# Optimization experiments

Hardware: AMD Instinct MI355X
Metric: run time of the kernel (lower is better)

Reference implementation:

```python
import jax, jax.numpy as jnp
import numpy as np

H = 256
K = 16
EPS_LN = 1e-5


def setup_inputs() -> dict:
    key = jax.random.key(0)
    ks = jax.random.split(key, 24)
    B, N = 64, 256
    s = lambda *sh: 1.0 / np.sqrt(sh[0])
    inp = {
        "feat": jax.random.normal(ks[0], (B, N, H), jnp.float32),
        "centers": jax.random.normal(ks[1], (B, N, 3), jnp.float32),
        "text_global": jax.random.normal(ks[2], (B, H), jnp.float32),
        # geom_mlp: Linear(4,H) -> ReLU -> Linear(H,H) -> ReLU
        "w_geom1": jax.random.normal(ks[3], (4, H), jnp.float32) * s(4),
        "b_geom1": jnp.zeros((H,), jnp.float32),
        "w_geom2": jax.random.normal(ks[4], (H, H), jnp.float32) * s(H),
        "b_geom2": jnp.zeros((H,), jnp.float32),
        # text gate / bias projections
        "w_gate": jax.random.normal(ks[5], (H, H), jnp.float32) * s(H),
        "b_gate": jnp.zeros((H,), jnp.float32),
        "w_tbias": jax.random.normal(ks[6], (H, H), jnp.float32) * s(H),
        "b_tbias": jnp.zeros((H,), jnp.float32),
        # edge_mlp: Linear(H,H//2) -> ReLU -> Linear(H//2,1)
        "w_edge1": jax.random.normal(ks[7], (H, H // 2), jnp.float32) * s(H),
        "b_edge1": jnp.zeros((H // 2,), jnp.float32),
        "w_edge2": jax.random.normal(ks[8], (H // 2, 1), jnp.float32) * s(H // 2),
        "b_edge2": jnp.zeros((1,), jnp.float32),
        # msg_mlp: Linear(H,H) -> ReLU
        "w_msg": jax.random.normal(ks[9], (H, H), jnp.float32) * s(H),
        "b_msg": jnp.zeros((H,), jnp.float32),
        # out_proj: Linear(2H,H) -> ReLU
        "w_out": jax.random.normal(ks[10], (2 * H, H), jnp.float32) * s(2 * H),
        "b_out": jnp.zeros((H,), jnp.float32),
        # LayerNorm params
        "ln_gamma": jnp.ones((H,), jnp.float32),
        "ln_beta": jnp.zeros((H,), jnp.float32),
    }
    return inp


def _forward(feat, centers, text_global,
             w_geom1, b_geom1, w_geom2, b_geom2,
             w_gate, b_gate, w_tbias, b_tbias,
             w_edge1, b_edge1, w_edge2, b_edge2,
             w_msg, b_msg, w_out, b_out, ln_gamma, ln_beta):
    B, N, Hd = feat.shape
    k = min(K, N)
    # pairwise euclidean distances (B,N,N)
    sq = jnp.sum(centers * centers, axis=-1)  # (B,N)
    d2 = sq[:, :, None] + sq[:, None, :] - 2.0 * jnp.einsum('bnc,bmc->bnm', centers, centers)
    dist_matrix = jnp.sqrt(jnp.maximum(d2, 0.0))
    # k smallest -> top_k of negated distances (sorted ascending in distance)
    _, knn_idx = jax.lax.top_k(-dist_matrix, k)  # (B,N,k)
    idx_flat = knn_idx.reshape(B, N * k)
    feat_neigh = jnp.take_along_axis(feat, idx_flat[:, :, None], axis=1).reshape(B, N, k, Hd)
    centers_neigh = jnp.take_along_axis(centers, idx_flat[:, :, None], axis=1).reshape(B, N, k, 3)
    rel = centers_neigh - centers[:, :, None, :]  # (B,N,k,3)
    dist = jnp.linalg.norm(rel, axis=-1, keepdims=True) + 1e-6
    geom = jnp.concatenate([rel, jnp.log1p(dist)], axis=-1)  # (B,N,k,4)
    geom_emb = jax.nn.relu(jax.nn.relu(geom @ w_geom1 + b_geom1) @ w_geom2 + b_geom2)
    text_gate = jax.nn.sigmoid(text_global @ w_gate + b_gate)[:, None, None, :]
    text_bias = (text_global @ w_tbias + b_tbias)[:, None, None, :]
    geom_cond = geom_emb * text_gate + text_bias
    edge_feat = jnp.tanh(feat[:, :, None, :] + feat_neigh + geom_cond)  # (B,N,k,H)
    edge_logits = (jax.nn.relu(edge_feat @ w_edge1 + b_edge1) @ w_edge2 + b_edge2)[..., 0]
    edge_alpha = jax.nn.softmax(edge_logits, axis=-1)[..., None]  # (B,N,k,1)
    msg = jax.nn.relu(feat_neigh @ w_msg + b_msg)
    ctx = jnp.sum(edge_alpha * msg, axis=2)  # (B,N,H)
    out = jax.nn.relu(jnp.concatenate([feat, ctx], axis=-1) @ w_out + b_out)
    x = feat + out
    mu = jnp.mean(x, axis=-1, keepdims=True)
    var = jnp.mean((x - mu) ** 2, axis=-1, keepdims=True)
    return (x - mu) / jnp.sqrt(var + EPS_LN) * ln_gamma + ln_beta


def reference(feat, centers, text_global,
              w_geom1, b_geom1, w_geom2, b_geom2,
              w_gate, b_gate, w_tbias, b_tbias,
              w_edge1, b_edge1, w_edge2, b_edge2,
              w_msg, b_msg, w_out, b_out, ln_gamma, ln_beta):
    return _forward(feat, centers, text_global,
                    w_geom1, b_geom1, w_geom2, b_geom2,
                    w_gate, b_gate, w_tbias, b_tbias,
                    w_edge1, b_edge1, w_edge2, b_edge2,
                    w_msg, b_msg, w_out, b_out, ln_gamma, ln_beta)
```

## Files before the change

kernel.cpp:

```cpp
#include <hip/hip_runtime.h>

#define H 256
#define KNN 16
#define NPT 256
#define BB 64

typedef unsigned short u16;
typedef unsigned int u32;
typedef __attribute__((ext_vector_type(8))) short shortx8;
typedef __attribute__((ext_vector_type(4))) float floatx4;

__device__ __forceinline__ u16 f2b(float f) {
    u32 u = __float_as_uint(f);
    u32 r = (u + 0x7fffu + ((u >> 16) & 1u)) >> 16;
    return (u16)r;
}

__device__ __forceinline__ float fast_tanh(float x) {
    float e = __builtin_amdgcn_exp2f(x * 2.88539008177793f);
    return 1.0f - 2.0f * __builtin_amdgcn_rcpf(e + 1.0f);
}

__global__ __launch_bounds__(256) void prep_kernel(
    const float* __restrict__ w2, const float* __restrict__ we1,
    const float* __restrict__ wm, const float* __restrict__ wo,
    const float* __restrict__ w1, const float* __restrict__ b1,
    u16* __restrict__ w2t, u16* __restrict__ we1t,
    u16* __restrict__ wmt, u16* __restrict__ wot, u16* __restrict__ w1t) {
    int tid = blockIdx.x * 256 + threadIdx.x;
    if (tid < 65536) {
        int n = tid >> 8, k = tid & 255;
        w2t[tid] = f2b(w2[k * 256 + n]);
    } else if (tid < 98304) {
        int t = tid - 65536;
        int n = t >> 8, k = t & 255;
        we1t[t] = f2b(we1[k * 128 + n]);
    } else if (tid < 163840) {
        int t = tid - 98304;
        int n = t >> 8, k = t & 255;
        wmt[t] = f2b(wm[k * 256 + n]);
    } else if (tid < 294912) {
        int t = tid - 163840;
        int n = t >> 9, k = t & 511;
        wot[t] = f2b(wo[k * 256 + n]);
    } else {
        int t = tid - 294912;
        int n = t >> 5, k = t & 31;
        float v = (k < 4) ? w1[k * 256 + n] : (k == 4 ? b1[n] : 0.0f);
        w1t[t] = f2b(v);
    }
}

__global__ __launch_bounds__(256) void knn_kernel(const float* __restrict__ centers,
                                                  int* __restrict__ knn) {
    __shared__ float cx[NPT], cy[NPT], cz[NPT], sq[NPT];
    __shared__ float dl[4][64][17];
    __shared__ int il[4][64][17];
    int blk = blockIdx.x;
    int b = blk >> 2, n0 = (blk & 3) * 64;
    int h = threadIdx.x;
    int s = h >> 6, pt = h & 63;
    {
        const float* cb = centers + (size_t)b * NPT * 3;
        float x = cb[h * 3 + 0], y = cb[h * 3 + 1], z = cb[h * 3 + 2];
        cx[h] = x; cy[h] = y; cz[h] = z;
        sq[h] = x * x + y * y + z * z;
    }
    __syncthreads();
    int n = n0 + pt;
    float x = cx[n], y = cy[n], z = cz[n], sn = sq[n];
    float bd[KNN];
    int bi[KNN];
#pragma unroll
    for (int j = 0; j < KNN; j++) { bd[j] = 1e30f; bi[j] = 0x7fffffff; }
    for (int mm = 0; mm < 64; mm++) {
        int m = s * 64 + mm;
        float dot = x * cx[m] + y * cy[m] + z * cz[m];
        float d2 = (sn + sq[m]) - 2.0f * dot;
        float d = sqrtf(fmaxf(d2, 0.0f));
        if (d < bd[KNN - 1]) {
            bd[KNN - 1] = d; bi[KNN - 1] = m;
#pragma unroll
            for (int p = KNN - 1; p > 0; --p) {
                if (bd[p - 1] > bd[p]) {
                    float td = bd[p - 1]; bd[p - 1] = bd[p]; bd[p] = td;
                    int ti = bi[p - 1]; bi[p - 1] = bi[p]; bi[p] = ti;
                }
            }
        }
    }
#pragma unroll
    for (int j = 0; j < KNN; j++) { dl[s][pt][j] = bd[j]; il[s][pt][j] = bi[j]; }
    __syncthreads();
    if (s == 0) {
        float md[KNN];
        int mi[KNN];
#pragma unroll
        for (int j = 0; j < KNN; j++) { md[j] = dl[0][pt][j]; mi[j] = il[0][pt][j]; }
        for (int t = 1; t < 4; t++) {
            for (int j = 0; j < KNN; j++) {
                float d = dl[t][pt][j];
                int idx = il[t][pt][j];
                bool ins = (d < md[KNN - 1]) || (d == md[KNN - 1] && idx < mi[KNN - 1]);
                if (!ins) break;
                md[KNN - 1] = d; mi[KNN - 1] = idx;
#pragma unroll
                for (int p = KNN - 1; p > 0; --p) {
                    bool sw = (md[p - 1] > md[p]) ||
                              (md[p - 1] == md[p] && mi[p - 1] > mi[p]);
                    if (sw) {
                        float td = md[p - 1]; md[p - 1] = md[p]; md[p] = td;
                        int ti = mi[p - 1]; mi[p - 1] = mi[p]; mi[p] = ti;
                    }
                }
            }
        }
        int* kp = knn + (b * NPT + n0 + pt) * KNN;
#pragma unroll
        for (int j = 0; j < KNN; j++) kp[j] = mi[j];
    }
}

__global__ __launch_bounds__(512) void gate_kernel(const float* __restrict__ tg_g,
                                                   const float* __restrict__ wg,
                                                   const float* __restrict__ bg,
                                                   const float* __restrict__ wtb,
                                                   const float* __restrict__ btb,
                                                   float* __restrict__ gate,
                                                   float* __restrict__ tbias) {
    __shared__ float tg[H];
    int b = blockIdx.x, t = threadIdx.x;
    if (t < H) tg[t] = tg_g[b * H + t];
    __syncthreads();
    int h = t & 255;
    if (t < H) {
        float ag = bg[h];
#pragma unroll 4
        for (int i = 0; i < H; i++) ag += tg[i] * wg[i * H + h];
        gate[b * H + h] = 1.0f / (1.0f + expf(-ag));
    } else {
        float ab = btb[h];
#pragma unroll 4
        for (int i = 0; i < H; i++) ab += tg[i] * wtb[i * H + h];
        tbias[b * H + h] = ab;
    }
}

__global__ __launch_bounds__(256, 4) void msg_mfma(const float* __restrict__ feat,
                                                   const u16* __restrict__ wmt,
                                                   const float* __restrict__ bm,
                                                   float* __restrict__ MSG) {
    __shared__ __attribute__((aligned(16))) u16 A[64][264];
    int p0 = blockIdx.x * 64, h = threadIdx.x;
    int w = h >> 6, lane = h & 63, quad = lane >> 4, lq = lane & 15;
#pragma unroll 8
    for (int row = 0; row < 64; row++)
        A[row][h] = f2b(feat[(size_t)(p0 + row) * H + h]);
    __syncthreads();
    floatx4 acc[4][4];
#pragma unroll
    for (int rt = 0; rt < 4; rt++)
#pragma unroll
        for (int ct = 0; ct < 4; ct++) acc[rt][ct] = (floatx4){0, 0, 0, 0};
#pragma unroll 2
    for (int kt = 0; kt < 8; kt++) {
        shortx8 bf[4];
#pragma unroll
        for (int ct = 0; ct < 4; ct++)
            bf[ct] = *(const shortx8*)&wmt[(w * 64 + ct * 16 + lq) * 256 + kt * 32 + quad * 8];
#pragma unroll
        for (int rt = 0; rt < 4; rt++) {
            shortx8 a = *(const shortx8*)&A[rt * 16 + lq][kt * 32 + quad * 8];
#pragma unroll
            for (int ct = 0; ct < 4; ct++)
                acc[rt][ct] = __builtin_amdgcn_mfma_f32_16x16x32_bf16(a, bf[ct], acc[rt][ct], 0, 0, 0);
        }
    }
#pragma unroll
    for (int ct = 0; ct < 4; ct++) {
        int col = w * 64 + ct * 16 + lq;
        float bmc = bm[col];
#pragma unroll
        for (int rt = 0; rt < 4; rt++)
#pragma unroll
            for (int r = 0; r < 4; r++) {
                int row = rt * 16 + quad * 4 + r;
                MSG[(size_t)(p0 + row) * H + col] = fmaxf(acc[rt][ct][r] + bmc, 0.0f);
            }
    }
}

__global__ __launch_bounds__(256, 4) void edge_mfma(
    const float* __restrict__ feat, const float* __restrict__ centers,
    const u16* __restrict__ w1t,
    const u16* __restrict__ w2t, const float* __restrict__ b2v,
    const u16* __restrict__ we1t, const float* __restrict__ be1,
    const float* __restrict__ we2, const float* __restrict__ be2,
    const int* __restrict__ knn, const float* __restrict__ gateG,
    const float* __restrict__ tbiasG, const float* __restrict__ MSG,
    float* __restrict__ ctxG) {
    __shared__ __attribute__((aligned(16))) u16 A[64][264];
    __shared__ float fnS[4][H];
    __shared__ __attribute__((aligned(16))) float geomS[64][4];
    __shared__ int nidxS[64];
    __shared__ float part[4][64];
    __shared__ float logitsS[64];
    __shared__ float alphaS[64];

    int bn0 = blockIdx.x * 4;
    int b = bn0 >> 8, n0 = bn0 & 255;
    int h = threadIdx.x;
    int w = h >> 6, lane = h & 63, quad = lane >> 4, lq = lane & 15;

    if (h < 64) nidxS[h] = knn[bn0 * KNN + h];
#pragma unroll
    for (int p = 0; p < 4; p++)
        fnS[p][h] = feat[(size_t)(bn0 + p) * H + h];
    if (h < 64) {
        int p = h >> 4;
        int m = nidxS[h];
        int n = n0 + p;
        const float* cb = centers + (size_t)b * NPT * 3;
        float rx = cb[m * 3 + 0] - cb[n * 3 + 0];
        float ry = cb[m * 3 + 1] - cb[n * 3 + 1];
        float rz = cb[m * 3 + 2] - cb[n * 3 + 2];
        float dist = sqrtf(rx * rx + ry * ry + rz * rz) + 1e-6f;
        geomS[h][0] = rx; geomS[h][1] = ry; geomS[h][2] = rz;
        geomS[h][3] = log1pf(dist);
    }
    __syncthreads();

    {
        shortx8 bw1[4];
#pragma unroll
        for (int ct = 0; ct < 4; ct++)
            bw1[ct] = *(const shortx8*)&w1t[(w * 64 + ct * 16 + lq) * 32 + quad * 8];
#pragma unroll
        for (int rt = 0; rt < 4; rt++) {
            shortx8 ag = {0, 0, 0, 0, 0, 0, 0, 0};
            if (quad == 0) {
                float4 g = *(const float4*)&geomS[rt * 16 + lq][0];
                ag[0] = (short)f2b(g.x);
                ag[1] = (short)f2b(g.y);
                ag[2] = (short)f2b(g.z);
                ag[3] = (short)f2b(g.w);
                ag[4] = (short)0x3F80;
            }
#pragma unroll
            for (int ct = 0; ct < 4; ct++) {
                floatx4 accg = __builtin_amdgcn_mfma_f32_16x16x32_bf16(
                    ag, bw1[ct], (floatx4){0, 0, 0, 0}, 0, 0, 0);
#pragma unroll
                for (int r = 0; r < 4; r++)
                    A[rt * 16 + quad * 4 + r][w * 64 + ct * 16 + lq] =
                        f2b(fmaxf(accg[r], 0.0f));
            }
        }
    }
    __syncthreads();

    floatx4 acc[4][4];
#pragma unroll
    for (int rt = 0; rt < 4; rt++)
#pragma unroll
        for (int ct = 0; ct < 4; ct++) acc[rt][ct] = (floatx4){0, 0, 0, 0};
#pragma unroll 2
    for (int kt = 0; kt < 8; kt++) {
        shortx8 bf[4];
#pragma unroll
        for (int ct = 0; ct < 4; ct++)
            bf[ct] = *(const shortx8*)&w2t[(w * 64 + ct * 16 + lq) * 256 + kt * 32 + quad * 8];
#pragma unroll
        for (int rt = 0; rt < 4; rt++) {
            shortx8 a = *(const shortx8*)&A[rt * 16 + lq][kt * 32 + quad * 8];
#pragma unroll
            for (int ct = 0; ct < 4; ct++)
                acc[rt][ct] = __builtin_amdgcn_mfma_f32_16x16x32_bf16(a, bf[ct], acc[rt][ct], 0, 0, 0);
        }
    }
    __syncthreads();

#pragma unroll
    for (int ct = 0; ct < 4; ct++) {
        int col = w * 64 + ct * 16 + lq;
        float b2c = b2v[col];
        float gc = gateG[b * H + col];
        float tc = tbiasG[b * H + col];
#pragma unroll
        for (int rt = 0; rt < 4; rt++) {
            float fnc = fnS[rt][col];
#pragma unroll
            for (int r = 0; r < 4; r++) {
                int row = rt * 16 + quad * 4 + r;
                float fb = feat[((size_t)b * NPT + nidxS[row]) * H + col];
                float emb = fmaxf(acc[rt][ct][r] + b2c, 0.0f);
                float ef = fast_tanh(fnc + fb + emb * gc + tc);
                A[row][col] = f2b(ef);
            }
        }
    }
    __syncthreads();

    floatx4 acc2[4][2];
#pragma unroll
    for (int rt = 0; rt < 4; rt++)
#pragma unroll
        for (int c2 = 0; c2 < 2; c2++) acc2[rt][c2] = (floatx4){0, 0, 0, 0};
#pragma unroll 2
    for (int kt = 0; kt < 8; kt++) {
        shortx8 bf[2];
#pragma unroll
        for (int c2 = 0; c2 < 2; c2++)
            bf[c2] = *(const shortx8*)&we1t[(w * 32 + c2 * 16 + lq) * 256 + kt * 32 + quad * 8];
#pragma unroll
        for (int rt = 0; rt < 4; rt++) {
            shortx8 a = *(const shortx8*)&A[rt * 16 + lq][kt * 32 + quad * 8];
#pragma unroll
            for (int c2 = 0; c2 < 2; c2++)
                acc2[rt][c2] = __builtin_amdgcn_mfma_f32_16x16x32_bf16(a, bf[c2], acc2[rt][c2], 0, 0, 0);
        }
    }

    float pl[4][4];
#pragma unroll
    for (int rt = 0; rt < 4; rt++)
#pragma unroll
        for (int r = 0; r < 4; r++) pl[rt][r] = 0.0f;
#pragma unroll
    for (int c2 = 0; c2 < 2; c2++) {
        int col = w * 32 + c2 * 16 + lq;
        float be1c = be1[col], w2c = we2[col];
#pragma unroll
        for (int rt = 0; rt < 4; rt++)
#pragma unroll
            for (int r = 0; r < 4; r++)
                pl[rt][r] += fmaxf(acc2[rt][c2][r] + be1c, 0.0f) * w2c;
    }
#pragma unroll
    for (int d = 1; d < 16; d <<= 1)
#pragma unroll
        for (int rt = 0; rt < 4; rt++)
#pragma unroll
            for (int r = 0; r < 4; r++) pl[rt][r] += __shfl_xor(pl[rt][r], d, 16);
    if (lq == 0) {
#pragma unroll
        for (int rt = 0; rt < 4; rt++)
#pragma unroll
            for (int r = 0; r < 4; r++)
                part[w][rt * 16 + quad * 4 + r] = pl[rt][r];
    }
    __syncthreads();
    if (h < 64)
        logitsS[h] = part[0][h] + part[1][h] + part[2][h] + part[3][h] + be2[0];
    __syncthreads();
    if (h < 64) {
        int base = (h >> 4) * 16;
        float mx = -1e30f;
#pragma unroll
        for (int j = 0; j < KNN; j++) mx = fmaxf(mx, logitsS[base + j]);
        float sum = 0.0f;
#pragma unroll
        for (int j = 0; j < KNN; j++) sum += expf(logitsS[base + j] - mx);
        alphaS[h] = expf(logitsS[h] - mx) / sum;
    }
    __syncthreads();

    {
        int p = h >> 6, cg = (h & 63) * 4;
        float4 c = {0, 0, 0, 0};
#pragma unroll
        for (int j = 0; j < KNN; j++) {
            float al = alphaS[p * 16 + j];
            float4 m = *(const float4*)&MSG[((size_t)b * NPT + nidxS[p * 16 + j]) * H + cg];
            c.x += al * m.x; c.y += al * m.y; c.z += al * m.z; c.w += al * m.w;
        }
        *(float4*)&ctxG[(size_t)(bn0 + p) * H + cg] = c;
    }
}

__global__ __launch_bounds__(256, 4) void out_mfma(const float* __restrict__ feat,
                                                   const float* __restrict__ ctxG,
                                                   const u16* __restrict__ wot,
                                                   const float* __restrict__ bo,
                                                   const float* __restrict__ gamma,
                                                   const float* __restrict__ beta,
                                                   float* __restrict__ out) {
    __shared__ __attribute__((aligned(16))) u16 A[32][520];
    __shared__ float redS[4][32], redS2[4][32];
    int p0 = blockIdx.x * 32, h = threadIdx.x;
    int w = h >> 6, lane = h & 63, quad = lane >> 4, lq = lane & 15;
#pragma unroll 8
    for (int row = 0; row < 32; row++) {
        A[row][h]       = f2b(feat[(size_t)(p0 + row) * H + h]);
        A[row][256 + h] = f2b(ctxG[(size_t)(p0 + row) * H + h]);
    }
    __syncthreads();
    floatx4 acc[2][4];
#pragma unroll
    for (int rt = 0; rt < 2; rt++)
#pragma unroll
        for (int ct = 0; ct < 4; ct++) acc[rt][ct] = (floatx4){0, 0, 0, 0};
#pragma unroll 2
    for (int kt = 0; kt < 16; kt++) {
        shortx8 bf[4];
#pragma unroll
        for (int ct = 0; ct < 4; ct++)
            bf[ct] = *(const shortx8*)&wot[(w * 64 + ct * 16 + lq) * 512 + kt * 32 + quad * 8];
#pragma unroll
        for (int rt = 0; rt < 2; rt++) {
            shortx8 a = *(const shortx8*)&A[rt * 16 + lq][kt * 32 + quad * 8];
#pragma unroll
            for (int ct = 0; ct < 4; ct++)
                acc[rt][ct] = __builtin_amdgcn_mfma_f32_16x16x32_bf16(a, bf[ct], acc[rt][ct], 0, 0, 0);
        }
    }
    float x[2][4][4];
    float sm[2][4], sq2[2][4];
#pragma unroll
    for (int rt = 0; rt < 2; rt++)
#pragma unroll
        for (int r = 0; r < 4; r++) { sm[rt][r] = 0.0f; sq2[rt][r] = 0.0f; }
#pragma unroll
    for (int rt = 0; rt < 2; rt++)
#pragma unroll
        for (int ct = 0; ct < 4; ct++) {
            int col = w * 64 + ct * 16 + lq;
            float boc = bo[col];
#pragma unroll
            for (int r = 0; r < 4; r++) {
                int row = rt * 16 + quad * 4 + r;
                float xx = feat[(size_t)(p0 + row) * H + col] +
                           fmaxf(acc[rt][ct][r] + boc, 0.0f);
                x[rt][ct][r] = xx;
                sm[rt][r] += xx;
                sq2[rt][r] += xx * xx;
            }
        }
#pragma unroll
    for (int d = 1; d < 16; d <<= 1)
#pragma unroll
        for (int rt = 0; rt < 2; rt++)
#pragma unroll
            for (int r = 0; r < 4; r++) {
                sm[rt][r] += __shfl_xor(sm[rt][r], d, 16);
                sq2[rt][r] += __shfl_xor(sq2[rt][r], d, 16);
            }
    if (lq == 0) {
#pragma unroll
        for (int rt = 0; rt < 2; rt++)
#pragma unroll
            for (int r = 0; r < 4; r++) {
                redS[w][rt * 16 + quad * 4 + r] = sm[rt][r];
                redS2[w][rt * 16 + quad * 4 + r] = sq2[rt][r];
            }
    }
    __syncthreads();
#pragma unroll
    for (int rt = 0; rt < 2; rt++)
#pragma unroll
        for (int r = 0; r < 4; r++) {
            int row = rt * 16 + quad * 4 + r;
            float s1 = redS[0][row] + redS[1][row] + redS[2][row] + redS[3][row];
            float s2 = redS2[0][row] + redS2[1][row] + redS2[2][row] + redS2[3][row];
            float mu = s1 * (1.0f / H);
            float var = s2 * (1.0f / H) - mu * mu;
            float inv = rsqrtf(fmaxf(var, 0.0f) + 1e-5f);
#pragma unroll
            for (int ct = 0; ct < 4; ct++) {
                int col = w * 64 + ct * 16 + lq;
                out[(size_t)(p0 + row) * H + col] =
                    (x[rt][ct][r] - mu) * inv * gamma[col] + beta[col];
            }
        }
}

extern "C" void kernel_launch(void* const* d_in, const int* in_sizes, int n_in,
                              void* d_out, int out_size, void* d_ws, size_t ws_size,
                              hipStream_t stream) {
    const float* feat    = (const float*)d_in[0];
    const float* centers = (const float*)d_in[1];
    const float* textg   = (const float*)d_in[2];
    const float* w1      = (const float*)d_in[3];
    const float* b1      = (const float*)d_in[4];
    const float* w2      = (const float*)d_in[5];
    const float* b2      = (const float*)d_in[6];
    const float* wg      = (const float*)d_in[7];
    const float* bg      = (const float*)d_in[8];
    const float* wtb     = (const float*)d_in[9];
    const float* btb     = (const float*)d_in[10];
    const float* we1     = (const float*)d_in[11];
    const float* be1     = (const float*)d_in[12];
    const float* we2     = (const float*)d_in[13];
    const float* be2     = (const float*)d_in[14];
    const float* wm      = (const float*)d_in[15];
    const float* bm      = (const float*)d_in[16];
    const float* wo      = (const float*)d_in[17];
    const float* bo      = (const float*)d_in[18];
    const float* gamma   = (const float*)d_in[19];
    const float* beta    = (const float*)d_in[20];

    char* ws = (char*)d_ws;
    size_t off = 0;
    int* knn     = (int*)(ws + off);   off += (size_t)BB * NPT * KNN * 4;
    float* gate  = (float*)(ws + off); off += (size_t)BB * H * 4;
    float* tbias = (float*)(ws + off); off += (size_t)BB * H * 4;
    float* MSG   = (float*)(ws + off); off += (size_t)BB * NPT * H * 4;
    float* ctxG  = (float*)(ws + off); off += (size_t)BB * NPT * H * 4;
    u16* w2t     = (u16*)(ws + off);   off += (size_t)256 * 256 * 2;
    u16* we1t    = (u16*)(ws + off);   off += (size_t)128 * 256 * 2;
    u16* wmt     = (u16*)(ws + off);   off += (size_t)256 * 256 * 2;
    u16* wot     = (u16*)(ws + off);   off += (size_t)256 * 512 * 2;
    u16* w1t     = (u16*)(ws + off);   off += (size_t)256 * 32 * 2;

    prep_kernel<<<1184, 256, 0, stream>>>(w2, we1, wm, wo, w1, b1,
                                          w2t, we1t, wmt, wot, w1t);
    knn_kernel<<<256, 256, 0, stream>>>(centers, knn);
    gate_kernel<<<BB, 512, 0, stream>>>(textg, wg, bg, wtb, btb, gate, tbias);
    msg_mfma<<<BB * NPT / 64, 256, 0, stream>>>(feat, wmt, bm, MSG);
    edge_mfma<<<BB * NPT / 4, 256, 0, stream>>>(feat, centers, w1t, w2t, b2,
                                                we1t, be1, we2, be2, knn, gate, tbias,
                                                MSG, ctxG);
    out_mfma<<<BB * NPT / 32, 256, 0, stream>>>(feat, ctxG, wot, bo, gamma, beta,
                                                (float*)d_out);
}
```

Before: 354.0 us.

## Store intermediates and feature copy in bf16 to halve memory traffic

Adds a bf16 copy of feat built in the prep kernel, and switches the MSG and ctx intermediate buffers from fp32 to bf16. The neighbour gathers in edge_mfma (feat and MSG rows) and the A-tile loads in msg_mfma and out_mfma now read half as many bytes. The aim is to cut global-memory and cache traffic on the gather-heavy edge kernel. It costs an extra pass over feat to convert it, and adds bf16 rounding to the neighbour features and the aggregated context.

Measured after the change: 347.3 us. About the same (-1.9%).

```diff
diff --git a/kernel.cpp b/kernel.cpp
--- a/kernel.cpp
+++ b/kernel.cpp
@@ -15,6 +15,9 @@
     u32 r = (u + 0x7fffu + ((u >> 16) & 1u)) >> 16;
     return (u16)r;
 }
+__device__ __forceinline__ float b2f(u16 u) {
+    return __uint_as_float(((u32)u) << 16);
+}
 
 __device__ __forceinline__ float fast_tanh(float x) {
     float e = __builtin_amdgcn_exp2f(x * 2.88539008177793f);
@@ -22,33 +25,45 @@
 }
 
 __global__ __launch_bounds__(256) void prep_kernel(
+    const float* __restrict__ feat,
     const float* __restrict__ w2, const float* __restrict__ we1,
     const float* __restrict__ wm, const float* __restrict__ wo,
     const float* __restrict__ w1, const float* __restrict__ b1,
     u16* __restrict__ w2t, u16* __restrict__ we1t,
-    u16* __restrict__ wmt, u16* __restrict__ wot, u16* __restrict__ w1t) {
-    int tid = blockIdx.x * 256 + threadIdx.x;
-    if (tid < 65536) {
-        int n = tid >> 8, k = tid & 255;
-        w2t[tid] = f2b(w2[k * 256 + n]);
-    } else if (tid < 98304) {
-        int t = tid - 65536;
-        int n = t >> 8, k = t & 255;
-        we1t[t] = f2b(we1[k * 128 + n]);
-    } else if (tid < 163840) {
-        int t = tid - 98304;
-        int n = t >> 8, k = t & 255;
-        wmt[t] = f2b(wm[k * 256 + n]);
-    } else if (tid < 294912) {
-        int t = tid - 163840;
-        int n = t >> 9, k = t & 511;
-        wot[t] = f2b(wo[k * 256 + n]);
-    } else {
-        int t = tid - 294912;
-        int n = t >> 5, k = t & 31;
-        float v = (k < 4) ? w1[k * 256 + n] : (k == 4 ? b1[n] : 0.0f);
-        w1t[t] = f2b(v);
-    }
+    u16* __restrict__ wmt, u16* __restrict__ wot, u16* __restrict__ w1t,
+    u16* __restrict__ featB) {
+    int blk = blockIdx.x;
+    if (blk < 1184) {
+        int tid = blk * 256 + threadIdx.x;
+        if (tid < 65536) {
+            int n = tid >> 8, k = tid & 255;
+            w2t[tid] = f2b(w2[k * 256 + n]);
+        } else if (tid < 98304) {
+            int t = tid - 65536;
+            int n = t >> 8, k = t & 255;
+            we1t[t] = f2b(we1[k * 128 + n]);
+        } else if (tid < 163840) {
+            int t = tid - 98304;
+            int n = t >> 8, k = t & 255;
+            wmt[t] = f2b(wm[k * 256 + n]);
+        } else if (tid < 294912) {
+            int t = tid - 163840;
+            int n = t >> 9, k = t & 511;
+            wot[t] = f2b(wo[k * 256 + n]);
+        } else {
+            int t = tid - 294912;
+            int n = t >> 5, k = t & 31;
+            float v = (k < 4) ? w1[k * 256 + n] : (k == 4 ? b1[n] : 0.0f);
+            w1t[t] = f2b(v);
+        }
+        return;
+    }
+    int e = (blk - 1184) * 256 + threadIdx.x;
+    float4 f = *(const float4*)&feat[(size_t)e * 4];
+    uint2 st;
+    st.x = (u32)f2b(f.x) | ((u32)f2b(f.y) << 16);
+    st.y = (u32)f2b(f.z) | ((u32)f2b(f.w) << 16);
+    *(uint2*)&featB[(size_t)e * 4] = st;
 }
 
 __global__ __launch_bounds__(256) void knn_kernel(const float* __restrict__ centers,
@@ -146,16 +161,16 @@
     }
 }
 
-__global__ __launch_bounds__(256, 4) void msg_mfma(const float* __restrict__ feat,
+__global__ __launch_bounds__(256, 4) void msg_mfma(const u16* __restrict__ featB,
                                                    const u16* __restrict__ wmt,
                                                    const float* __restrict__ bm,
-                                                   float* __restrict__ MSG) {
+                                                   u16* __restrict__ MSGB) {
     __shared__ __attribute__((aligned(16))) u16 A[64][264];
     int p0 = blockIdx.x * 64, h = threadIdx.x;
     int w = h >> 6, lane = h & 63, quad = lane >> 4, lq = lane & 15;
 #pragma unroll 8
     for (int row = 0; row < 64; row++)
-        A[row][h] = f2b(feat[(size_t)(p0 + row) * H + h]);
+        A[row][h] = featB[(size_t)(p0 + row) * H + h];
     __syncthreads();
     floatx4 acc[4][4];
 #pragma unroll
@@ -185,20 +200,21 @@
 #pragma unroll
             for (int r = 0; r < 4; r++) {
                 int row = rt * 16 + quad * 4 + r;
-                MSG[(size_t)(p0 + row) * H + col] = fmaxf(acc[rt][ct][r] + bmc, 0.0f);
+                MSGB[(size_t)(p0 + row) * H + col] = f2b(fmaxf(acc[rt][ct][r] + bmc, 0.0f));
             }
     }
 }
 
 __global__ __launch_bounds__(256, 4) void edge_mfma(
-    const float* __restrict__ feat, const float* __restrict__ centers,
+    const float* __restrict__ feat, const u16* __restrict__ featB,
+    const float* __restrict__ centers,
     const u16* __restrict__ w1t,
     const u16* __restrict__ w2t, const float* __restrict__ b2v,
     const u16* __restrict__ we1t, const float* __restrict__ be1,
     const float* __restrict__ we2, const float* __restrict__ be2,
     const int* __restrict__ knn, const float* __restrict__ gateG,
-    const float* __restrict__ tbiasG, const float* __restrict__ MSG,
-    float* __restrict__ ctxG) {
+    const float* __restrict__ tbiasG, const u16* __restrict__ MSGB,
+    u16* __restrict__ ctxB) {
     __shared__ __attribute__((aligned(16))) u16 A[64][264];
     __shared__ float fnS[4][H];
     __shared__ __attribute__((aligned(16))) float geomS[64][4];
@@ -292,7 +308,7 @@
 #pragma unroll
             for (int r = 0; r < 4; r++) {
                 int row = rt * 16 + quad * 4 + r;
-                float fb = feat[((size_t)b * NPT + nidxS[row]) * H + col];
+                float fb = b2f(featB[((size_t)b * NPT + nidxS[row]) * H + col]);
                 float emb = fmaxf(acc[rt][ct][r] + b2c, 0.0f);
                 float ef = fast_tanh(fnc + fb + emb * gc + tc);
                 A[row][col] = f2b(ef);
@@ -371,15 +387,23 @@
 #pragma unroll
         for (int j = 0; j < KNN; j++) {
             float al = alphaS[p * 16 + j];
-            float4 m = *(const float4*)&MSG[((size_t)b * NPT + nidxS[p * 16 + j]) * H + cg];
-            c.x += al * m.x; c.y += al * m.y; c.z += al * m.z; c.w += al * m.w;
-        }
-        *(float4*)&ctxG[(size_t)(bn0 + p) * H + cg] = c;
+            const u32* mp = (const u32*)&MSGB[((size_t)b * NPT + nidxS[p * 16 + j]) * H + cg];
+            u32 m0 = mp[0], m1 = mp[1];
+            c.x += al * __uint_as_float(m0 << 16);
+            c.y += al * __uint_as_float(m0 & 0xFFFF0000u);
+            c.z += al * __uint_as_float(m1 << 16);
+            c.w += al * __uint_as_float(m1 & 0xFFFF0000u);
+        }
+        uint2 st;
+        st.x = (u32)f2b(c.x) | ((u32)f2b(c.y) << 16);
+        st.y = (u32)f2b(c.z) | ((u32)f2b(c.w) << 16);
+        *(uint2*)&ctxB[(size_t)(bn0 + p) * H + cg] = st;
     }
 }
 
 __global__ __launch_bounds__(256, 4) void out_mfma(const float* __restrict__ feat,
-                                                   const float* __restrict__ ctxG,
+                                                   const u16* __restrict__ featB,
+                                                   const u16* __restrict__ ctxB,
                                                    const u16* __restrict__ wot,
                                                    const float* __restrict__ bo,
                                                    const float* __restrict__ gamma,
@@ -391,8 +415,8 @@
     int w = h >> 6, lane = h & 63, quad = lane >> 4, lq = lane & 15;
 #pragma unroll 8
     for (int row = 0; row < 32; row++) {
-        A[row][h]       = f2b(feat[(size_t)(p0 + row) * H + h]);
-        A[row][256 + h] = f2b(ctxG[(size_t)(p0 + row) * H + h]);
+        A[row][h]       = featB[(size_t)(p0 + row) * H + h];
+        A[row][256 + h] = ctxB[(size_t)(p0 + row) * H + h];
     }
     __syncthreads();
     floatx4 acc[2][4];
@@ -504,22 +528,23 @@
     int* knn     = (int*)(ws + off);   off += (size_t)BB * NPT * KNN * 4;
     float* gate  = (float*)(ws + off); off += (size_t)BB * H * 4;
     float* tbias = (float*)(ws + off); off += (size_t)BB * H * 4;
-    float* MSG   = (float*)(ws + off); off += (size_t)BB * NPT * H * 4;
-    float* ctxG  = (float*)(ws + off); off += (size_t)BB * NPT * H * 4;
+    u16* MSGB    = (u16*)(ws + off);   off += (size_t)BB * NPT * H * 2;
+    u16* ctxB    = (u16*)(ws + off);   off += (size_t)BB * NPT * H * 2;
+    u16* featB   = (u16*)(ws + off);   off += (size_t)BB * NPT * H * 2;
     u16* w2t     = (u16*)(ws + off);   off += (size_t)256 * 256 * 2;
     u16* we1t    = (u16*)(ws + off);   off += (size_t)128 * 256 * 2;
     u16* wmt     = (u16*)(ws + off);   off += (size_t)256 * 256 * 2;
     u16* wot     = (u16*)(ws + off);   off += (size_t)256 * 512 * 2;
     u16* w1t     = (u16*)(ws + off);   off += (size_t)256 * 32 * 2;
 
-    prep_kernel<<<1184, 256, 0, stream>>>(w2, we1, wm, wo, w1, b1,
-                                          w2t, we1t, wmt, wot, w1t);
+    prep_kernel<<<5280, 256, 0, stream>>>(feat, w2, we1, wm, wo, w1, b1,
+                                          w2t, we1t, wmt, wot, w1t, featB);
     knn_kernel<<<256, 256, 0, stream>>>(centers, knn);
     gate_kernel<<<BB, 512, 0, stream>>>(textg, wg, bg, wtb, btb, gate, tbias);
-    msg_mfma<<<BB * NPT / 64, 256, 0, stream>>>(feat, wmt, bm, MSG);
-    edge_mfma<<<BB * NPT / 4, 256, 0, stream>>>(feat, centers, w1t, w2t, b2,
+    msg_mfma<<<BB * NPT / 64, 256, 0, stream>>>(featB, wmt, bm, MSGB);
+    edge_mfma<<<BB * NPT / 4, 256, 0, stream>>>(feat, featB, centers, w1t, w2t, b2,
                                                 we1t, be1, we2, be2, knn, gate, tbias,
-                                                MSG, ctxG);
-    out_mfma<<<BB * NPT / 32, 256, 0, stream>>>(feat, ctxG, wot, bo, gamma, beta,
-                                                (float*)d_out);
-}
+                                                MSGB, ctxB);
+    out_mfma<<<BB * NPT / 32, 256, 0, stream>>>(feat, featB, ctxB, wot, bo,
+                                                gamma, beta, (float*)d_out);
+}
```
